# Kernel optimization log

Measured on AMD Instinct MI355X. Metric: run time of the kernel, lower is better.

The kernel has to match this reference:

```python
import jax, jax.numpy as jnp
import numpy as np

N_NODES = 100000
N_EDGES = 1600000
IN_F = 128
C1, C2, C3 = 32, 64, 64
HEADS, GAT_CH = 4, 16  # concat -> 64
NEG_SLOPE = 0.2  # PyG GATConv default leaky_relu slope


def _add_self_loops(src, dst, n):
    loop = jnp.arange(n, dtype=src.dtype)
    return jnp.concatenate([src, loop]), jnp.concatenate([dst, loop])


def gcn_conv(x, src, dst, W, b, n):
    # PyG GCNConv: D^{-1/2} (A + I) D^{-1/2} X W + b  (self-loops already in src/dst)
    h = x @ W
    deg = jax.ops.segment_sum(jnp.ones_like(dst, dtype=h.dtype), dst, num_segments=n)
    dinv = jnp.where(deg > 0, jax.lax.rsqrt(deg), 0.0)
    norm = dinv[src] * dinv[dst]                              # [E]
    out = jax.ops.segment_sum(h[src] * norm[:, None], dst, num_segments=n)
    return out + b


def gat_conv(x, src, dst, W, att_src, att_dst, b, n):
    # PyG GATConv (concat=True), self-loops already in src/dst
    h = (x @ W).reshape(n, HEADS, GAT_CH)                     # [N,H,C]
    a_s = jnp.sum(h * att_src, axis=-1)                       # [N,H]
    a_d = jnp.sum(h * att_dst, axis=-1)                       # [N,H]
    e = jax.nn.leaky_relu(a_s[src] + a_d[dst], NEG_SLOPE)     # [E,H]
    # segment softmax over incoming edges of each dst node
    emax = jax.ops.segment_max(e, dst, num_segments=n)
    ex = jnp.exp(e - emax[dst])
    denom = jax.ops.segment_sum(ex, dst, num_segments=n)
    alpha = ex / (denom[dst] + 1e-16)                         # [E,H]
    out = jax.ops.segment_sum(h[src] * alpha[:, :, None], dst, num_segments=n)
    return out.reshape(n, HEADS * GAT_CH) + b


def setup_inputs() -> dict:
    key = jax.random.key(0)
    ks = jax.random.split(key, 16)
    x = jax.random.normal(ks[0], (N_NODES, IN_F), dtype=jnp.float32)
    edge_index = jax.random.randint(ks[1], (2, N_EDGES), 0, N_NODES, dtype=jnp.int32)
    s = 0.1
    return {
        "x": x,
        "edge_index": edge_index,
        "W1": jax.random.normal(ks[2], (IN_F, C1), jnp.float32) * s,
        "b1": jnp.zeros((C1,), jnp.float32),
        "W2": jax.random.normal(ks[3], (C1, C2), jnp.float32) * s,
        "b2": jnp.zeros((C2,), jnp.float32),
        "W3": jax.random.normal(ks[4], (C3, C3), jnp.float32) * s,
        "b3": jnp.zeros((C3,), jnp.float32),
        "Wg": jax.random.normal(ks[5], (C2, HEADS * GAT_CH), jnp.float32) * s,
        "att_src": jax.random.normal(ks[6], (HEADS, GAT_CH), jnp.float32) * s,
        "att_dst": jax.random.normal(ks[7], (HEADS, GAT_CH), jnp.float32) * s,
        "bg": jnp.zeros((HEADS * GAT_CH,), jnp.float32),
        "Wl": jax.random.normal(ks[8], (HEADS * GAT_CH, 1), jnp.float32) * s,
        "bl": jnp.zeros((1,), jnp.float32),
    }


def reference(x, edge_index, W1, b1, W2, b2, W3, b3, Wg, att_src, att_dst, bg, Wl, bl):
    n = x.shape[0]
    src, dst = _add_self_loops(edge_index[0], edge_index[1], n)
    h = jax.nn.relu(gcn_conv(x, src, dst, W1, b1, n))           # dropout = identity (eval)
    h = jax.nn.relu(gcn_conv(h, src, dst, W2, b2, n))
    h = jax.nn.relu(gat_conv(h, src, dst, Wg, att_src, att_dst, bg, n))
    h_res = jax.nn.relu(gcn_conv(h, src, dst, W3, b3, n))
    h = h + h_res
    h = jax.nn.relu(gat_conv(h, src, dst, Wg, att_src, att_dst, bg, n))
    return jax.nn.relu(h @ Wl + bl)                              # [N,1]
```

## Files before the change

kernel.cpp:

```cpp
#include <hip/hip_runtime.h>
#include <math.h>

constexpr int KIN = 128;

typedef _Float16 half8_t __attribute__((ext_vector_type(8)));
typedef _Float16 half4_t __attribute__((ext_vector_type(4)));


__global__ void rx_hist(const int* __restrict__ dst, int* __restrict__ hist_g,
                        int E, int CH, int NB, int NBKT) {
    __shared__ int h[256];
    int b = blockIdx.x;
    for (int i = threadIdx.x; i < 256; i += blockDim.x) h[i] = 0;
    __syncthreads();
    int beg = b * CH, end = min(beg + CH, E);
    for (int e = beg + threadIdx.x; e < end; e += blockDim.x)
        atomicAdd(&h[dst[e] >> 9], 1);
    __syncthreads();
    for (int d = threadIdx.x; d < NBKT; d += blockDim.x)
        hist_g[d * NB + b] = h[d];
}

__global__ void gs_reduce(const int* __restrict__ a, int* __restrict__ bsum, int m) {
    __shared__ int s[256];
    int t = threadIdx.x;
    int i = blockIdx.x * 256 + t;
    s[t] = (i < m) ? a[i] : 0;
    __syncthreads();
    for (int off = 128; off > 0; off >>= 1) {
        if (t < off) s[t] += s[t + off];
        __syncthreads();
    }
    if (t == 0) bsum[blockIdx.x] = s[0];
}

__global__ void gs_blocksums(const int* __restrict__ bsum, int* __restrict__ bpre, int nb) {
    __shared__ int s[512];
    int t = threadIdx.x;
    int val = (t < nb) ? bsum[t] : 0;
    s[t] = val;
    __syncthreads();
    for (int off = 1; off < 512; off <<= 1) {
        int x = (t >= off) ? s[t - off] : 0;
        __syncthreads();
        s[t] += x;
        __syncthreads();
    }
    if (t < nb) bpre[t] = s[t] - val;
}

__global__ void gs_scatter(const int* __restrict__ a, const int* __restrict__ bpre,
                           int* __restrict__ out, int m) {
    __shared__ int s[256];
    int t = threadIdx.x;
    int i = blockIdx.x * 256 + t;
    int val = (i < m) ? a[i] : 0;
    s[t] = val;
    __syncthreads();
    for (int off = 1; off < 256; off <<= 1) {
        int x = (t >= off) ? s[t - off] : 0;
        __syncthreads();
        s[t] += x;
        __syncthreads();
    }
    if (i < m) out[i] = bpre[blockIdx.x] + s[t] - val;
}

__global__ void rx_scatter(const int* __restrict__ src, const int* __restrict__ dst,
                           const int* __restrict__ excl, int* __restrict__ s1,
                           int* __restrict__ d1, int E, int CH, int NB, int NBKT) {
    __shared__ int offs[256];
    int b = blockIdx.x;
    for (int d = threadIdx.x; d < NBKT; d += blockDim.x)
        offs[d] = excl[d * NB + b];
    __syncthreads();
    int beg = b * CH, end = min(beg + CH, E);
    for (int e = beg + threadIdx.x; e < end; e += blockDim.x) {
        int dd = dst[e];
        int pos = atomicAdd(&offs[dd >> 9], 1);
        s1[pos] = src[e];
        d1[pos] = dd;
    }
}

__global__ void __launch_bounds__(512)
bucket_sort(const int* __restrict__ s1, const int* __restrict__ d1,
            const int* __restrict__ excl, int* __restrict__ csr,
            int* __restrict__ row_ptr, float* __restrict__ dinv,
            int E, int NB, int NBKT, int n) {
    __shared__ int hist[512];
    __shared__ int scan[512];
    __shared__ int offs[512];
    int b = blockIdx.x, t = threadIdx.x;
    int base = excl[b * NB];
    int endb = (b + 1 < NBKT) ? excl[(b + 1) * NB] : E;
    hist[t] = 0;
    __syncthreads();
    for (int i = base + t; i < endb; i += 512)
        atomicAdd(&hist[d1[i] & 511], 1);
    __syncthreads();
    int v = hist[t];
    scan[t] = v;
    __syncthreads();
    for (int off = 1; off < 512; off <<= 1) {
        int x = (t >= off) ? scan[t - off] : 0;
        __syncthreads();
        scan[t] += x;
        __syncthreads();
    }
    int ex = scan[t] - v;
    offs[t] = ex;
    int node = b * 512 + t;
    if (node < n) {
        row_ptr[node] = base + ex;
        dinv[node] = 1.0f / sqrtf((float)(v + 1));
    }
    if (b == NBKT - 1 && t == 0) row_ptr[n] = E;
    __syncthreads();
    for (int i = base + t; i < endb; i += 512) {
        int dd = d1[i];
        int pos = atomicAdd(&offs[dd & 511], 1);
        csr[base + pos] = s1[i];
    }
}

template <int K, int F, int BM, int THREADS, bool SCALE, bool BRELU, bool ATT, bool OUT16>
__global__ void __launch_bounds__(THREADS)
gemm_tile(const float* __restrict__ in, const float* __restrict__ W,
          const float* __restrict__ dinv, const float* __restrict__ bias,
          const float* __restrict__ att_src, const float* __restrict__ att_dst,
          float* __restrict__ a_s, float* __restrict__ a_d,
          float* __restrict__ out, int n) {
    constexpr int TM = 4, TN = 4;
    constexpr int TX = F / TN;
    constexpr int TY = BM / TM;
    static_assert(THREADS == TX * TY, "thread count mismatch");
    constexpr int K4 = K / 4;
    __shared__ float xs[K][BM];
    __shared__ float Ws[K * F];
    int t = threadIdx.x;
    int row0 = blockIdx.x * BM;

    for (int i = t; i < K * F / 4; i += THREADS)
        ((float4*)Ws)[i] = ((const float4*)W)[i];

    for (int i = t; i < BM * K4; i += THREADS) {
        int r = i % BM, k4 = i / BM;
        int row = row0 + r;
        float4 v = {0.f, 0.f, 0.f, 0.f};
        if (row < n) v = ((const float4*)(in + (size_t)row * K))[k4];
        xs[4 * k4 + 0][r] = v.x;
        xs[4 * k4 + 1][r] = v.y;
        xs[4 * k4 + 2][r] = v.z;
        xs[4 * k4 + 3][r] = v.w;
    }
    __syncthreads();

    int tx = t % TX, ty = t / TX;
    float acc[TM][TN] = {};
#pragma unroll 4
    for (int k = 0; k < K; ++k) {
        float4 xv = *(const float4*)&xs[k][ty * TM];
        float4 wv = *(const float4*)&Ws[k * F + tx * TN];
        float xr[4] = {xv.x, xv.y, xv.z, xv.w};
        float wr[4] = {wv.x, wv.y, wv.z, wv.w};
#pragma unroll
        for (int i = 0; i < TM; ++i)
#pragma unroll
            for (int j = 0; j < TN; ++j)
                acc[i][j] = fmaf(xr[i], wr[j], acc[i][j]);
    }

#pragma unroll
    for (int i = 0; i < TM; ++i) {
        int row = row0 + ty * TM + i;
        if (row >= n) continue;
        float s = SCALE ? dinv[row] : 1.0f;
        float o[4];
        if (BRELU) {
            o[0] = fmaxf(fmaf(acc[i][0], s, bias[4 * tx + 0]), 0.f);
            o[1] = fmaxf(fmaf(acc[i][1], s, bias[4 * tx + 1]), 0.f);
            o[2] = fmaxf(fmaf(acc[i][2], s, bias[4 * tx + 2]), 0.f);
            o[3] = fmaxf(fmaf(acc[i][3], s, bias[4 * tx + 3]), 0.f);
        } else {
            o[0] = acc[i][0] * s; o[1] = acc[i][1] * s;
            o[2] = acc[i][2] * s; o[3] = acc[i][3] * s;
        }
        if (OUT16) {
            half4_t oh;
            oh[0] = (_Float16)o[0]; oh[1] = (_Float16)o[1];
            oh[2] = (_Float16)o[2]; oh[3] = (_Float16)o[3];
            *(half4_t*)((_Float16*)out + (size_t)row * F + 4 * tx) = oh;
        } else {
            float4 of = {o[0], o[1], o[2], o[3]};
            ((float4*)(out + (size_t)row * F))[tx] = of;
        }
    }
    if (ATT) {
        int hd = tx >> 2;
        float as0 = att_src[4 * tx + 0], as1 = att_src[4 * tx + 1];
        float as2 = att_src[4 * tx + 2], as3 = att_src[4 * tx + 3];
        float ad0 = att_dst[4 * tx + 0], ad1 = att_dst[4 * tx + 1];
        float ad2 = att_dst[4 * tx + 2], ad3 = att_dst[4 * tx + 3];
#pragma unroll
        for (int i = 0; i < TM; ++i) {
            float ps = acc[i][0] * as0 + acc[i][1] * as1 + acc[i][2] * as2 + acc[i][3] * as3;
            float pd = acc[i][0] * ad0 + acc[i][1] * ad1 + acc[i][2] * ad2 + acc[i][3] * ad3;
            ps += __shfl_xor(ps, 1); pd += __shfl_xor(pd, 1);
            ps += __shfl_xor(ps, 2); pd += __shfl_xor(pd, 2);
            int row = row0 + ty * TM + i;
            if ((tx & 3) == 0 && row < n) {
                a_s[row * 4 + hd] = ps;
                a_d[row * 4 + hd] = pd;
            }
        }
    }
}

__global__ void __launch_bounds__(256)
gemm2_gat(const float* __restrict__ T, const float* __restrict__ W2,
          const float* __restrict__ b2, const float* __restrict__ dinv,
          const float* __restrict__ Wg, const float* __restrict__ att_src,
          const float* __restrict__ att_dst, float* __restrict__ a_s,
          float* __restrict__ a_d, float* __restrict__ A1, int n) {
    __shared__ float xs[32][64];
    __shared__ float W2s[32 * 64];
    __shared__ float Wgs[64 * 64];
    __shared__ float hs[64][68];
    int t = threadIdx.x;
    int row0 = blockIdx.x * 64;

    for (int i = t; i < 32 * 64 / 4; i += 256) ((float4*)W2s)[i] = ((const float4*)W2)[i];
    for (int i = t; i < 64 * 64 / 4; i += 256) ((float4*)Wgs)[i] = ((const float4*)Wg)[i];
    for (int i = t; i < 64 * 8; i += 256) {
        int r = i % 64, k4 = i / 64;
        int row = row0 + r;
        float4 v = {0.f, 0.f, 0.f, 0.f};
        if (row < n) v = ((const float4*)(T + (size_t)row * 32))[k4];
        xs[4 * k4 + 0][r] = v.x;
        xs[4 * k4 + 1][r] = v.y;
        xs[4 * k4 + 2][r] = v.z;
        xs[4 * k4 + 3][r] = v.w;
    }
    __syncthreads();

    int tx = t % 16, ty = t / 16;
    {
        float acc[4][4] = {};
#pragma unroll 4
        for (int k = 0; k < 32; ++k) {
            float4 xv = *(const float4*)&xs[k][ty * 4];
            float4 wv = *(const float4*)&W2s[k * 64 + tx * 4];
            float xr[4] = {xv.x, xv.y, xv.z, xv.w};
            float wr[4] = {wv.x, wv.y, wv.z, wv.w};
#pragma unroll
            for (int i = 0; i < 4; ++i)
#pragma unroll
                for (int j = 0; j < 4; ++j)
                    acc[i][j] = fmaf(xr[i], wr[j], acc[i][j]);
        }
#pragma unroll
        for (int i = 0; i < 4; ++i) {
            int row = row0 + ty * 4 + i;
            float s = (row < n) ? dinv[row] : 0.f;
#pragma unroll
            for (int j = 0; j < 4; ++j)
                hs[4 * tx + j][ty * 4 + i] = fmaxf(fmaf(acc[i][j], s, b2[4 * tx + j]), 0.f);
        }
    }
    __syncthreads();

    float acc[4][4] = {};
#pragma unroll 4
    for (int k = 0; k < 64; ++k) {
        float4 xv = *(const float4*)&hs[k][ty * 4];
        float4 wv = *(const float4*)&Wgs[k * 64 + tx * 4];
        float xr[4] = {xv.x, xv.y, xv.z, xv.w};
        float wr[4] = {wv.x, wv.y, wv.z, wv.w};
#pragma unroll
        for (int i = 0; i < 4; ++i)
#pragma unroll
            for (int j = 0; j < 4; ++j)
                acc[i][j] = fmaf(xr[i], wr[j], acc[i][j]);
    }
    _Float16* A1h = (_Float16*)A1;
#pragma unroll
    for (int i = 0; i < 4; ++i) {
        int row = row0 + ty * 4 + i;
        if (row >= n) continue;
        half4_t oh;
        oh[0] = (_Float16)acc[i][0]; oh[1] = (_Float16)acc[i][1];
        oh[2] = (_Float16)acc[i][2]; oh[3] = (_Float16)acc[i][3];
        *(half4_t*)(A1h + (size_t)row * 64 + 4 * tx) = oh;
    }
    {
        int hd = tx >> 2;
        float as0 = att_src[4 * tx + 0], as1 = att_src[4 * tx + 1];
        float as2 = att_src[4 * tx + 2], as3 = att_src[4 * tx + 3];
        float ad0 = att_dst[4 * tx + 0], ad1 = att_dst[4 * tx + 1];
        float ad2 = att_dst[4 * tx + 2], ad3 = att_dst[4 * tx + 3];
#pragma unroll
        for (int i = 0; i < 4; ++i) {
            float ps = acc[i][0] * as0 + acc[i][1] * as1 + acc[i][2] * as2 + acc[i][3] * as3;
            float pd = acc[i][0] * ad0 + acc[i][1] * ad1 + acc[i][2] * ad2 + acc[i][3] * ad3;
            ps += __shfl_xor(ps, 1); pd += __shfl_xor(pd, 1);
            ps += __shfl_xor(ps, 2); pd += __shfl_xor(pd, 2);
            int row = row0 + ty * 4 + i;
            if ((tx & 3) == 0 && row < n) {
                a_s[row * 4 + hd] = ps;
                a_d[row * 4 + hd] = pd;
            }
        }
    }
}

template <int MODE>
__global__ void __launch_bounds__(256)
gcn_agg_h32(const _Float16* __restrict__ Hs, const int* __restrict__ row_ptr,
            const int* __restrict__ csr, const float* __restrict__ dinv,
            const float* __restrict__ bias, void* __restrict__ outp, int n) {
    int idx = blockIdx.x * blockDim.x + threadIdx.x;
    int v = idx >> 6;
    int lane = idx & 63;
    if (v >= n) return;
    int cg = lane & 3;
    int slot = lane >> 2;
    const half8_t* H8 = (const half8_t*)Hs;

    float acc[8] = {};
    if (slot == 0) {
        half8_t h = H8[(size_t)v * 4 + cg];
#pragma unroll
        for (int j = 0; j < 8; ++j) acc[j] = (float)h[j];
    }
    int beg = row_ptr[v], end = row_ptr[v + 1];
    int iters = (end - beg + 15) >> 4;
    int e = beg + slot;
    bool val = e < end;
    int u = val ? csr[e] : v;
    half8_t h = H8[(size_t)u * 4 + cg];
    for (int i = 0; i < iters; ++i) {
        int en = e + 16;
        bool valn = en < end;
        int un = valn ? csr[en] : v;
        half8_t hn = H8[(size_t)un * 4 + cg];
        float m = val ? 1.f : 0.f;
#pragma unroll
        for (int j = 0; j < 8; ++j) acc[j] = fmaf(m, (float)h[j], acc[j]);
        e = en; val = valn; h = hn;
    }
#pragma unroll
    for (int off = 4; off < 64; off <<= 1) {
#pragma unroll
        for (int j = 0; j < 8; ++j) acc[j] += __shfl_xor(acc[j], off);
    }
    if (slot == 0) {
        if (MODE == 1) {
            float dv = dinv[v];
            half8_t o;
#pragma unroll
            for (int j = 0; j < 8; ++j)
                o[j] = (_Float16)(dv * fmaxf(fmaf(dv, acc[j], bias[8 * cg + j]), 0.f));
            ((half8_t*)outp)[(size_t)v * 4 + cg] = o;
        } else {
            float* of = (float*)outp;
            float4 o0 = {acc[0], acc[1], acc[2], acc[3]};
            float4 o1 = {acc[4], acc[5], acc[6], acc[7]};
            float4* dst4 = (float4*)(of + (size_t)v * 32 + 8 * cg);
            dst4[0] = o0;
            dst4[1] = o1;
        }
    }
}

__global__ void __launch_bounds__(256)
gcn_agg_h64(const _Float16* __restrict__ Hs, const int* __restrict__ row_ptr,
            const int* __restrict__ csr, const float* __restrict__ dinv,
            const float* __restrict__ bias, const float* __restrict__ res,
            float* __restrict__ out, int n) {
    int idx = blockIdx.x * blockDim.x + threadIdx.x;
    int v = idx >> 6;
    int lane = idx & 63;
    if (v >= n) return;
    int cg = lane & 7;
    int slot = lane >> 3;
    const half8_t* H8 = (const half8_t*)Hs;

    float acc[8] = {};
    if (slot == 0) {
        half8_t h = H8[(size_t)v * 8 + cg];
#pragma unroll
        for (int j = 0; j < 8; ++j) acc[j] = (float)h[j];
    }
    int beg = row_ptr[v], end = row_ptr[v + 1];
    int iters = (end - beg + 7) >> 3;
    int e = beg + slot;
    bool val = e < end;
    int u = val ? csr[e] : v;
    half8_t h = H8[(size_t)u * 8 + cg];
    for (int i = 0; i < iters; ++i) {
        int en = e + 8;
        bool valn = en < end;
        int un = valn ? csr[en] : v;
        half8_t hn = H8[(size_t)un * 8 + cg];
        float m = val ? 1.f : 0.f;
#pragma unroll
        for (int j = 0; j < 8; ++j) acc[j] = fmaf(m, (float)h[j], acc[j]);
        e = en; val = valn; h = hn;
    }
#pragma unroll
    for (int off = 8; off < 64; off <<= 1) {
#pragma unroll
        for (int j = 0; j < 8; ++j) acc[j] += __shfl_xor(acc[j], off);
    }
    if (slot == 0) {
        float dv = dinv[v];
        const float4* r4 = (const float4*)(res + (size_t)v * 64 + 8 * cg);
        float4 r0 = r4[0], r1 = r4[1];
        float o[8];
#pragma unroll
        for (int j = 0; j < 8; ++j)
            o[j] = fmaxf(fmaf(dv, acc[j], bias[8 * cg + j]), 0.f);
        float4 o0 = {o[0] + r0.x, o[1] + r0.y, o[2] + r0.z, o[3] + r0.w};
        float4 o1 = {o[4] + r1.x, o[5] + r1.y, o[6] + r1.z, o[7] + r1.w};
        float4* dst4 = (float4*)(out + (size_t)v * 64 + 8 * cg);
        dst4[0] = o0;
        dst4[1] = o1;
    }
}

template <bool FINAL>
__global__ void __launch_bounds__(256)
gat_agg_h(const _Float16* __restrict__ H, const int* __restrict__ row_ptr,
          const int* __restrict__ csr, const float* __restrict__ a_s,
          const float* __restrict__ a_d, const float* __restrict__ bias,
          const float* __restrict__ Wl, const float* __restrict__ bl,
          float* __restrict__ out, int n) {
    int idx = blockIdx.x * blockDim.x + threadIdx.x;
    int v = idx >> 6;
    int lane = idx & 63;
    if (v >= n) return;
    int cg = lane & 7;
    int slot = lane >> 3;
    int hd = cg >> 1;
    const half8_t* H8 = (const half8_t*)H;

    float adv = a_d[v * 4 + hd];
    float l = 0.f;
    float acc[8] = {};
    if (slot == 0) {
        float e0 = a_s[v * 4 + hd] + adv;
        e0 = fmaxf(e0, 0.2f * e0);
        float p = __expf(e0);
        l = p;
        half8_t h = H8[(size_t)v * 8 + cg];
#pragma unroll
        for (int j = 0; j < 8; ++j) acc[j] = p * (float)h[j];
    }
    int beg = row_ptr[v], end = row_ptr[v + 1];
    int iters = (end - beg + 7) >> 3;
    int e = beg + slot;
    bool val = e < end;
    int u = val ? csr[e] : v;
    half8_t h = H8[(size_t)u * 8 + cg];
    float as = a_s[u * 4 + hd];
    for (int i = 0; i < iters; ++i) {
        int en = e + 8;
        bool valn = en < end;
        int un = valn ? csr[en] : v;
        half8_t hn = H8[(size_t)un * 8 + cg];
        float asn = a_s[un * 4 + hd];
        float ev = as + adv;
        ev = fmaxf(ev, 0.2f * ev);
        float p = val ? __expf(ev) : 0.f;
        l += p;
#pragma unroll
        for (int j = 0; j < 8; ++j) acc[j] = fmaf(p, (float)h[j], acc[j]);
        e = en; val = valn; h = hn; as = asn;
    }
#pragma unroll
    for (int off = 8; off < 64; off <<= 1) {
        l += __shfl_xor(l, off);
#pragma unroll
        for (int j = 0; j < 8; ++j) acc[j] += __shfl_xor(acc[j], off);
    }
    float rl = 1.0f / (l + 1e-16f);
    if (!FINAL) {
        if (slot == 0) {
            float o[8];
#pragma unroll
            for (int j = 0; j < 8; ++j)
                o[j] = fmaxf(fmaf(acc[j], rl, bias[8 * cg + j]), 0.f);
            float4 o0 = {o[0], o[1], o[2], o[3]};
            float4 o1 = {o[4], o[5], o[6], o[7]};
            float4* dst4 = (float4*)(out + (size_t)v * 64 + 8 * cg);
            dst4[0] = o0;
            dst4[1] = o1;
        }
    } else {
        float p = 0.f;
#pragma unroll
        for (int j = 0; j < 8; ++j)
            p += fmaxf(fmaf(acc[j], rl, bias[8 * cg + j]), 0.f) * Wl[8 * cg + j];
        p += __shfl_xor(p, 1);
        p += __shfl_xor(p, 2);
        p += __shfl_xor(p, 4);
        if (lane == 0) out[v] = fmaxf(p + bl[0], 0.f);
    }
}


extern "C" void kernel_launch(void* const* d_in, const int* in_sizes, int n_in,
                              void* d_out, int out_size, void* d_ws, size_t ws_size,
                              hipStream_t stream) {
    const float* x     = (const float*)d_in[0];
    const int*   ei    = (const int*)d_in[1];
    const float* W1    = (const float*)d_in[2];
    const float* b1    = (const float*)d_in[3];
    const float* W2    = (const float*)d_in[4];
    const float* b2    = (const float*)d_in[5];
    const float* W3    = (const float*)d_in[6];
    const float* b3    = (const float*)d_in[7];
    const float* Wg    = (const float*)d_in[8];
    const float* att_s = (const float*)d_in[9];
    const float* att_d = (const float*)d_in[10];
    const float* bg    = (const float*)d_in[11];
    const float* Wl    = (const float*)d_in[12];
    const float* bl    = (const float*)d_in[13];
    float* out = (float*)d_out;

    int n = in_sizes[0] / KIN;
    int E = in_sizes[1] / 2;
    const int* srcp = ei;
    const int* dstp = ei + E;

    int NB = 128;
    int CH = (E + NB - 1) / NB;
    int NBKT = (n + 511) >> 9;
    int M = NBKT * NB;

    char* w = (char*)d_ws;
    auto alloc = [&](size_t bytes) -> void* {
        void* p = (void*)w;
        w += (bytes + 255) & ~(size_t)255;
        return p;
    };
    int*   row_ptr = (int*)alloc((size_t)(n + 1) * 4);
    int*   csr     = (int*)alloc((size_t)E * 4);
    int*   hist_g  = (int*)alloc((size_t)M * 4);
    int*   excl    = (int*)alloc((size_t)M * 4);
    int*   bsum    = (int*)alloc(512 * 4);
    int*   bpre    = (int*)alloc(512 * 4);
    float* dinv    = (float*)alloc((size_t)n * 4);
    float* a_s     = (float*)alloc((size_t)n * 4 * 4);
    float* a_d     = (float*)alloc((size_t)n * 4 * 4);
    float* bufA    = (float*)alloc((size_t)n * 64 * 4);
    float* bufB    = (float*)alloc((size_t)n * 64 * 4);
    float* bufC    = (float*)alloc((size_t)n * 64 * 4);
    int* s1 = (int*)bufB;
    int* d1 = ((int*)bufB) + E;

    int msb = (M + 255) / 256;
    rx_hist<<<NB, 256, 0, stream>>>(dstp, hist_g, E, CH, NB, NBKT);
    gs_reduce<<<msb, 256, 0, stream>>>(hist_g, bsum, M);
    gs_blocksums<<<1, 512, 0, stream>>>(bsum, bpre, msb);
    gs_scatter<<<msb, 256, 0, stream>>>(hist_g, bpre, excl, M);
    rx_scatter<<<NB, 256, 0, stream>>>(srcp, dstp, excl, s1, d1, E, CH, NB, NBKT);
    bucket_sort<<<NBKT, 512, 0, stream>>>(s1, d1, excl, csr, row_ptr, dinv, E, NB, NBKT, n);

    int agg_blocks = (n * 64 + 255) / 256;
    int gemm_blocks = (n + 63) / 64;

    gemm_tile<128, 32, 64, 128, true, false, false, true><<<gemm_blocks, 128, 0, stream>>>(
        x, W1, dinv, nullptr, nullptr, nullptr, nullptr, nullptr, bufA, n);
    gcn_agg_h32<1><<<agg_blocks, 256, 0, stream>>>(
        (const _Float16*)bufA, row_ptr, csr, dinv, b1, bufB, n);
    gcn_agg_h32<2><<<agg_blocks, 256, 0, stream>>>(
        (const _Float16*)bufB, row_ptr, csr, nullptr, nullptr, bufA, n);
    gemm2_gat<<<gemm_blocks, 256, 0, stream>>>(bufA, W2, b2, dinv, Wg, att_s, att_d, a_s, a_d, bufB, n);
    gat_agg_h<false><<<agg_blocks, 256, 0, stream>>>(
        (const _Float16*)bufB, row_ptr, csr, a_s, a_d, bg, nullptr, nullptr, bufC, n);
    gemm_tile<64, 64, 64, 256, true, false, false, true><<<gemm_blocks, 256, 0, stream>>>(
        bufC, W3, dinv, nullptr, nullptr, nullptr, nullptr, nullptr, bufA, n);
    gcn_agg_h64<<<agg_blocks, 256, 0, stream>>>(
        (const _Float16*)bufA, row_ptr, csr, dinv, b3, bufC, bufB, n);
    gemm_tile<64, 64, 64, 256, false, false, true, true><<<gemm_blocks, 256, 0, stream>>>(
        bufB, Wg, nullptr, nullptr, att_s, att_d, a_s, a_d, bufA, n);
    gat_agg_h<true><<<agg_blocks, 256, 0, stream>>>(
        (const _Float16*)bufA, row_ptr, csr, a_s, a_d, bg, Wl, bl, out, n);
}
```

Measured before the change: 507.4 us.

## Pad CSR rows to multiples of 16 with a zero sentinel node

```diff
diff --git a/kernel.cpp b/kernel.cpp
--- a/kernel.cpp
+++ b/kernel.cpp
@@ -122,6 +122,28 @@
         int pos = atomicAdd(&offs[dd & 511], 1);
         csr[base + pos] = s1[i];
     }
+}
+
+__global__ void pad_deg(const int* __restrict__ row_ptr, int* __restrict__ pd, int n) {
+    int v = blockIdx.x * 256 + threadIdx.x;
+    if (v < n) {
+        int d = row_ptr[v + 1] - row_ptr[v];
+        int p = (d + 15) & ~15;
+        pd[v] = (p < 16) ? 16 : p;
+    }
+}
+
+__global__ void pad_copy(const int* __restrict__ row_ptr, const int* __restrict__ rpp,
+                         const int* __restrict__ pd, const int* __restrict__ csr,
+                         int* __restrict__ csr_pad, int n) {
+    int idx = blockIdx.x * blockDim.x + threadIdx.x;
+    int v = idx >> 6;
+    int lane = idx & 63;
+    if (v >= n) return;
+    int beg = row_ptr[v], deg = row_ptr[v + 1] - beg;
+    int begp = rpp[v], pdeg = pd[v];
+    for (int i = lane; i < pdeg; i += 64)
+        csr_pad[begp + i] = (i < deg) ? csr[beg + i] : n;
 }
 
 template <int K, int F, int BM, int THREADS, bool SCALE, bool BRELU, bool ATT, bool OUT16>
@@ -174,6 +196,12 @@
 #pragma unroll
     for (int i = 0; i < TM; ++i) {
         int row = row0 + ty * TM + i;
+        if (OUT16 && row == n) {
+            half4_t z;
+            z[0] = (_Float16)0.f; z[1] = (_Float16)0.f;
+            z[2] = (_Float16)0.f; z[3] = (_Float16)0.f;
+            *(half4_t*)((_Float16*)out + (size_t)row * F + 4 * tx) = z;
+        }
         if (row >= n) continue;
         float s = SCALE ? dinv[row] : 1.0f;
         float o[4];
@@ -209,9 +237,14 @@
             ps += __shfl_xor(ps, 1); pd += __shfl_xor(pd, 1);
             ps += __shfl_xor(ps, 2); pd += __shfl_xor(pd, 2);
             int row = row0 + ty * TM + i;
-            if ((tx & 3) == 0 && row < n) {
-                a_s[row * 4 + hd] = ps;
-                a_d[row * 4 + hd] = pd;
+            if ((tx & 3) == 0) {
+                if (row < n) {
+                    a_s[row * 4 + hd] = ps;
+                    a_d[row * 4 + hd] = pd;
+                } else if (row == n) {
+                    a_s[row * 4 + hd] = -1e30f;
+                    a_d[row * 4 + hd] = 0.f;
+                }
             }
         }
     }
@@ -287,6 +320,12 @@
 #pragma unroll
     for (int i = 0; i < 4; ++i) {
         int row = row0 + ty * 4 + i;
+        if (row == n) {
+            half4_t z;
+            z[0] = (_Float16)0.f; z[1] = (_Float16)0.f;
+            z[2] = (_Float16)0.f; z[3] = (_Float16)0.f;
+            *(half4_t*)(A1h + (size_t)row * 64 + 4 * tx) = z;
+        }
         if (row >= n) continue;
         half4_t oh;
         oh[0] = (_Float16)acc[i][0]; oh[1] = (_Float16)acc[i][1];
@@ -306,9 +345,14 @@
             ps += __shfl_xor(ps, 1); pd += __shfl_xor(pd, 1);
             ps += __shfl_xor(ps, 2); pd += __shfl_xor(pd, 2);
             int row = row0 + ty * 4 + i;
-            if ((tx & 3) == 0 && row < n) {
-                a_s[row * 4 + hd] = ps;
-                a_d[row * 4 + hd] = pd;
+            if ((tx & 3) == 0) {
+                if (row < n) {
+                    a_s[row * 4 + hd] = ps;
+                    a_d[row * 4 + hd] = pd;
+                } else if (row == n) {
+                    a_s[row * 4 + hd] = -1e30f;
+                    a_d[row * 4 + hd] = 0.f;
+                }
             }
         }
     }
@@ -316,39 +360,47 @@
 
 template <int MODE>
 __global__ void __launch_bounds__(256)
-gcn_agg_h32(const _Float16* __restrict__ Hs, const int* __restrict__ row_ptr,
-            const int* __restrict__ csr, const float* __restrict__ dinv,
-            const float* __restrict__ bias, void* __restrict__ outp, int n) {
+gcn_agg_h32(const _Float16* __restrict__ Hs, const int* __restrict__ rpp,
+            const int* __restrict__ pd, const int* __restrict__ csr_pad,
+            const float* __restrict__ dinv, const float* __restrict__ bias,
+            void* __restrict__ outp, int n) {
     int idx = blockIdx.x * blockDim.x + threadIdx.x;
     int v = idx >> 6;
     int lane = idx & 63;
-    if (v >= n) return;
+    if (v >= n) {
+        if (MODE == 1 && v == n && lane < 4) {
+            half8_t z;
+#pragma unroll
+            for (int j = 0; j < 8; ++j) z[j] = (_Float16)0.f;
+            ((half8_t*)outp)[(size_t)n * 4 + lane] = z;
+        }
+        return;
+    }
     int cg = lane & 3;
     int slot = lane >> 2;
     const half8_t* H8 = (const half8_t*)Hs;
 
     float acc[8] = {};
     if (slot == 0) {
-        half8_t h = H8[(size_t)v * 4 + cg];
+        half8_t h = H8[v * 4 + cg];
 #pragma unroll
         for (int j = 0; j < 8; ++j) acc[j] = (float)h[j];
     }
-    int beg = row_ptr[v], end = row_ptr[v + 1];
-    int iters = (end - beg + 15) >> 4;
-    int e = beg + slot;
-    bool val = e < end;
-    int u = val ? csr[e] : v;
-    half8_t h = H8[(size_t)u * 4 + cg];
-    for (int i = 0; i < iters; ++i) {
-        int en = e + 16;
-        bool valn = en < end;
-        int un = valn ? csr[en] : v;
-        half8_t hn = H8[(size_t)un * 4 + cg];
-        float m = val ? 1.f : 0.f;
-#pragma unroll
-        for (int j = 0; j < 8; ++j) acc[j] = fmaf(m, (float)h[j], acc[j]);
-        e = en; val = valn; h = hn;
-    }
+    int begp = rpp[v];
+    int iters = pd[v] >> 4;
+    int e = begp + slot;
+    int u = csr_pad[e];
+    half8_t h = H8[u * 4 + cg];
+    for (int i = 1; i < iters; ++i) {
+        e += 16;
+        int un = csr_pad[e];
+        half8_t hn = H8[un * 4 + cg];
+#pragma unroll
+        for (int j = 0; j < 8; ++j) acc[j] += (float)h[j];
+        h = hn;
+    }
+#pragma unroll
+    for (int j = 0; j < 8; ++j) acc[j] += (float)h[j];
 #pragma unroll
     for (int off = 4; off < 64; off <<= 1) {
 #pragma unroll
@@ -374,10 +426,10 @@
 }
 
 __global__ void __launch_bounds__(256)
-gcn_agg_h64(const _Float16* __restrict__ Hs, const int* __restrict__ row_ptr,
-            const int* __restrict__ csr, const float* __restrict__ dinv,
-            const float* __restrict__ bias, const float* __restrict__ res,
-            float* __restrict__ out, int n) {
+gcn_agg_h64(const _Float16* __restrict__ Hs, const int* __restrict__ rpp,
+            const int* __restrict__ pd, const int* __restrict__ csr_pad,
+            const float* __restrict__ dinv, const float* __restrict__ bias,
+            const float* __restrict__ res, float* __restrict__ out, int n) {
     int idx = blockIdx.x * blockDim.x + threadIdx.x;
     int v = idx >> 6;
     int lane = idx & 63;
@@ -388,26 +440,25 @@
 
     float acc[8] = {};
     if (slot == 0) {
-        half8_t h = H8[(size_t)v * 8 + cg];
+        half8_t h = H8[v * 8 + cg];
 #pragma unroll
         for (int j = 0; j < 8; ++j) acc[j] = (float)h[j];
     }
-    int beg = row_ptr[v], end = row_ptr[v + 1];
-    int iters = (end - beg + 7) >> 3;
-    int e = beg + slot;
-    bool val = e < end;
-    int u = val ? csr[e] : v;
-    half8_t h = H8[(size_t)u * 8 + cg];
-    for (int i = 0; i < iters; ++i) {
-        int en = e + 8;
-        bool valn = en < end;
-        int un = valn ? csr[en] : v;
-        half8_t hn = H8[(size_t)un * 8 + cg];
-        float m = val ? 1.f : 0.f;
-#pragma unroll
-        for (int j = 0; j < 8; ++j) acc[j] = fmaf(m, (float)h[j], acc[j]);
-        e = en; val = valn; h = hn;
-    }
+    int begp = rpp[v];
+    int iters = pd[v] >> 3;
+    int e = begp + slot;
+    int u = csr_pad[e];
+    half8_t h = H8[u * 8 + cg];
+    for (int i = 1; i < iters; ++i) {
+        e += 8;
+        int un = csr_pad[e];
+        half8_t hn = H8[un * 8 + cg];
+#pragma unroll
+        for (int j = 0; j < 8; ++j) acc[j] += (float)h[j];
+        h = hn;
+    }
+#pragma unroll
+    for (int j = 0; j < 8; ++j) acc[j] += (float)h[j];
 #pragma unroll
     for (int off = 8; off < 64; off <<= 1) {
 #pragma unroll
@@ -431,11 +482,11 @@
 
 template <bool FINAL>
 __global__ void __launch_bounds__(256)
-gat_agg_h(const _Float16* __restrict__ H, const int* __restrict__ row_ptr,
-          const int* __restrict__ csr, const float* __restrict__ a_s,
-          const float* __restrict__ a_d, const float* __restrict__ bias,
-          const float* __restrict__ Wl, const float* __restrict__ bl,
-          float* __restrict__ out, int n) {
+gat_agg_h(const _Float16* __restrict__ H, const int* __restrict__ rpp,
+          const int* __restrict__ pd, const int* __restrict__ csr_pad,
+          const float* __restrict__ a_s, const float* __restrict__ a_d,
+          const float* __restrict__ bias, const float* __restrict__ Wl,
+          const float* __restrict__ bl, float* __restrict__ out, int n) {
     int idx = blockIdx.x * blockDim.x + threadIdx.x;
     int v = idx >> 6;
     int lane = idx & 63;
@@ -453,30 +504,36 @@
         e0 = fmaxf(e0, 0.2f * e0);
         float p = __expf(e0);
         l = p;
-        half8_t h = H8[(size_t)v * 8 + cg];
+        half8_t h = H8[v * 8 + cg];
 #pragma unroll
         for (int j = 0; j < 8; ++j) acc[j] = p * (float)h[j];
     }
-    int beg = row_ptr[v], end = row_ptr[v + 1];
-    int iters = (end - beg + 7) >> 3;
-    int e = beg + slot;
-    bool val = e < end;
-    int u = val ? csr[e] : v;
-    half8_t h = H8[(size_t)u * 8 + cg];
+    int begp = rpp[v];
+    int iters = pd[v] >> 3;
+    int e = begp + slot;
+    int u = csr_pad[e];
+    half8_t h = H8[u * 8 + cg];
     float as = a_s[u * 4 + hd];
-    for (int i = 0; i < iters; ++i) {
-        int en = e + 8;
-        bool valn = en < end;
-        int un = valn ? csr[en] : v;
-        half8_t hn = H8[(size_t)un * 8 + cg];
+    for (int i = 1; i < iters; ++i) {
+        e += 8;
+        int un = csr_pad[e];
+        half8_t hn = H8[un * 8 + cg];
         float asn = a_s[un * 4 + hd];
         float ev = as + adv;
         ev = fmaxf(ev, 0.2f * ev);
-        float p = val ? __expf(ev) : 0.f;
+        float p = __expf(ev);
         l += p;
 #pragma unroll
         for (int j = 0; j < 8; ++j) acc[j] = fmaf(p, (float)h[j], acc[j]);
-        e = en; val = valn; h = hn; as = asn;
+        h = hn; as = asn;
+    }
+    {
+        float ev = as + adv;
+        ev = fmaxf(ev, 0.2f * ev);
+        float p = __expf(ev);
+        l += p;
+#pragma unroll
+        for (int j = 0; j < 8; ++j) acc[j] = fmaf(p, (float)h[j], acc[j]);
     }
 #pragma unroll
     for (int off = 8; off < 64; off <<= 1) {
@@ -546,17 +603,20 @@
         return p;
     };
     int*   row_ptr = (int*)alloc((size_t)(n + 1) * 4);
-    int*   csr     = (int*)alloc((size_t)E * 4);
     int*   hist_g  = (int*)alloc((size_t)M * 4);
     int*   excl    = (int*)alloc((size_t)M * 4);
     int*   bsum    = (int*)alloc(512 * 4);
     int*   bpre    = (int*)alloc(512 * 4);
     float* dinv    = (float*)alloc((size_t)n * 4);
-    float* a_s     = (float*)alloc((size_t)n * 4 * 4);
-    float* a_d     = (float*)alloc((size_t)n * 4 * 4);
+    float* a_s     = (float*)alloc((size_t)(n + 1) * 4 * 4);
+    float* a_d     = (float*)alloc((size_t)(n + 1) * 4 * 4);
     float* bufA    = (float*)alloc((size_t)n * 64 * 4);
     float* bufB    = (float*)alloc((size_t)n * 64 * 4);
     float* bufC    = (float*)alloc((size_t)n * 64 * 4);
+    int*   pdv     = (int*)alloc((size_t)n * 4);
+    int*   rpp     = (int*)alloc((size_t)n * 4);
+    int*   csr_pad = (int*)alloc(((size_t)E + 16 * (size_t)n + 64) * 4);
+    int* csr = (int*)bufC;
     int* s1 = (int*)bufB;
     int* d1 = ((int*)bufB) + E;
 
@@ -568,24 +628,31 @@
     rx_scatter<<<NB, 256, 0, stream>>>(srcp, dstp, excl, s1, d1, E, CH, NB, NBKT);
     bucket_sort<<<NBKT, 512, 0, stream>>>(s1, d1, excl, csr, row_ptr, dinv, E, NB, NBKT, n);
 
-    int agg_blocks = (n * 64 + 255) / 256;
+    int msbn = (n + 255) / 256;
+    pad_deg<<<msbn, 256, 0, stream>>>(row_ptr, pdv, n);
+    gs_reduce<<<msbn, 256, 0, stream>>>(pdv, bsum, n);
+    gs_blocksums<<<1, 512, 0, stream>>>(bsum, bpre, msbn);
+    gs_scatter<<<msbn, 256, 0, stream>>>(pdv, bpre, rpp, n);
+    pad_copy<<<(n * 64 + 255) / 256, 256, 0, stream>>>(row_ptr, rpp, pdv, csr, csr_pad, n);
+
+    int agg_blocks = ((n + 1) * 64 + 255) / 256;
     int gemm_blocks = (n + 63) / 64;
 
     gemm_tile<128, 32, 64, 128, true, false, false, true><<<gemm_blocks, 128, 0, stream>>>(
         x, W1, dinv, nullptr, nullptr, nullptr, nullptr, nullptr, bufA, n);
     gcn_agg_h32<1><<<agg_blocks, 256, 0, stream>>>(
-        (const _Float16*)bufA, row_ptr, csr, dinv, b1, bufB, n);
+        (const _Float16*)bufA, rpp, pdv, csr_pad, dinv, b1, bufB, n);
     gcn_agg_h32<2><<<agg_blocks, 256, 0, stream>>>(
-        (const _Float16*)bufB, row_ptr, csr, nullptr, nullptr, bufA, n);
+        (const _Float16*)bufB, rpp, pdv, csr_pad, nullptr, nullptr, bufA, n);
     gemm2_gat<<<gemm_blocks, 256, 0, stream>>>(bufA, W2, b2, dinv, Wg, att_s, att_d, a_s, a_d, bufB, n);
     gat_agg_h<false><<<agg_blocks, 256, 0, stream>>>(
-        (const _Float16*)bufB, row_ptr, csr, a_s, a_d, bg, nullptr, nullptr, bufC, n);
+        (const _Float16*)bufB, rpp, pdv, csr_pad, a_s, a_d, bg, nullptr, nullptr, bufC, n);
     gemm_tile<64, 64, 64, 256, true, false, false, true><<<gemm_blocks, 256, 0, stream>>>(
         bufC, W3, dinv, nullptr, nullptr, nullptr, nullptr, nullptr, bufA, n);
     gcn_agg_h64<<<agg_blocks, 256, 0, stream>>>(
-        (const _Float16*)bufA, row_ptr, csr, dinv, b3, bufC, bufB, n);
+        (const _Float16*)bufA, rpp, pdv, csr_pad, dinv, b3, bufC, bufB, n);
     gemm_tile<64, 64, 64, 256, false, false, true, true><<<gemm_blocks, 256, 0, stream>>>(
         bufB, Wg, nullptr, nullptr, att_s, att_d, a_s, a_d, bufA, n);
     gat_agg_h<true><<<agg_blocks, 256, 0, stream>>>(
-        (const _Float16*)bufA, row_ptr, csr, a_s, a_d, bg, Wl, bl, out, n);
-}
+        (const _Float16*)bufA, rpp, pdv, csr_pad, a_s, a_d, bg, Wl, bl, out, n);
+}
```

After: 533.5 us. 1.05x slower.
